# Performance work log

Hardware: AMD Instinct MI355X
Metric: run time of the kernel (lower is better)

Reference implementation:

```python
import jax, jax.numpy as jnp
import numpy as np

EPS = 1e-5

def conv2d(x, w, pad):
    # x: NCHW, w: OIHW, stride 1, symmetric padding
    return jax.lax.conv_general_dilated(
        x, w, window_strides=(1, 1), padding=[(pad, pad), (pad, pad)],
        dimension_numbers=('NCHW', 'OIHW', 'NCHW'))

def bn_eval(x, gamma, beta, mean, var):
    # eval-mode BatchNorm2d: per-channel affine with running stats
    s = gamma / jnp.sqrt(var + EPS)
    return x * s[None, :, None, None] + (beta - mean * s)[None, :, None, None]

def setup_inputs() -> dict:
    key = jax.random.key(0)
    ks = jax.random.split(key, 12)
    B, Cin, C, H, W = 2, 6, 64, 512, 512
    R, K = 4, 5                 # res_num, ksize
    Cf = 2 * 3 * K              # ch_out_final = 30
    d = {}
    d['feature_map'] = jax.random.normal(ks[0], (B, Cin, H, W), jnp.float32)
    d['base'] = jax.random.normal(ks[1], (B, 3, H, W), jnp.float32)
    d['w_first'] = jax.random.normal(ks[2], (C, Cin, 7, 7), jnp.float32) * 0.05
    d['kb_w1'] = jax.random.normal(ks[3], (R, C, C, 3, 3), jnp.float32) * 0.05
    d['kb_g1'] = jnp.ones((R, C), jnp.float32)
    d['kb_b1'] = jnp.zeros((R, C), jnp.float32)
    d['kb_m1'] = jax.random.normal(ks[4], (R, C), jnp.float32) * 0.1
    d['kb_v1'] = jax.random.uniform(ks[5], (R, C), jnp.float32) + 0.5
    d['kb_w2'] = jax.random.normal(ks[6], (R, C, C, 3, 3), jnp.float32) * 0.05
    d['kb_g2'] = jnp.ones((R, C), jnp.float32)
    d['kb_b2'] = jnp.zeros((R, C), jnp.float32)
    d['kb_m2'] = jax.random.normal(ks[7], (R, C), jnp.float32) * 0.1
    d['kb_v2'] = jax.random.uniform(ks[8], (R, C), jnp.float32) + 0.5
    d['w_last'] = jax.random.normal(ks[9], (Cf, C, 3, 3), jnp.float32) * 0.05
    return d

def reference(feature_map, base, w_first, kb_w1, kb_g1, kb_b1, kb_m1, kb_v1,
              kb_w2, kb_g2, kb_b2, kb_m2, kb_v2, w_last):
    K = 5
    P = K // 2
    b, _, h, w = base.shape
    # conv_first: 7x7 conv + ReLU
    y = jax.nn.relu(conv2d(feature_map, w_first, 3))
    # residual KB blocks: (conv3x3 -> BN -> ReLU) x2 + skip
    R = kb_w1.shape[0]
    for i in range(R):
        t = jax.nn.relu(bn_eval(conv2d(y, kb_w1[i], 1), kb_g1[i], kb_b1[i], kb_m1[i], kb_v1[i]))
        t = jax.nn.relu(bn_eval(conv2d(t, kb_w2[i], 1), kb_g2[i], kb_b2[i], kb_m2[i], kb_v2[i]))
        y = t + y
    # conv_last: [b, 2*3*K, h, w]
    y = conv2d(y, w_last, 1)
    Cf = y.shape[1]
    # [b,3,2K,h,w] -> [b,3,h,w,2K]
    weight = y.reshape(b, 3, Cf // 3, h, w).transpose(0, 1, 3, 4, 2)
    weight_h = jax.nn.softmax(weight[..., :K], axis=-1)  # [b,3,h,w,K]
    weight_w = jax.nn.softmax(weight[..., K:], axis=-1)
    # vertical adaptive filtering: pad H by P, unfold along H
    pad_h = jnp.pad(base, ((0, 0), (0, 0), (P, P), (0, 0)))
    unf_h = jnp.stack([pad_h[:, :, i:i + h, :] for i in range(K)], axis=-1)  # [b,3,h,w,K]
    filt_h = (unf_h * weight_h).sum(axis=-1)  # [b,3,h,w]
    # horizontal adaptive filtering: pad W by P, unfold along W
    pad_w = jnp.pad(filt_h, ((0, 0), (0, 0), (0, 0), (P, P)))
    unf_w = jnp.stack([pad_w[:, :, :, i:i + w] for i in range(K)], axis=-1)  # [b,3,h,w,K]
    return (unf_w * weight_w).sum(axis=-1)
```

## Files before the change

kernel.cpp:

```cpp
#include <hip/hip_runtime.h>
#include <math.h>

typedef __attribute__((ext_vector_type(8)))  short short8;
typedef __attribute__((ext_vector_type(4)))  float float4v;
typedef __attribute__((ext_vector_type(16))) float f32x16;

__device__ __forceinline__ unsigned short f2bf(float f) {
    union { float f; unsigned u; } x; x.f = f;
    unsigned r = x.u + 0x7FFFu + ((x.u >> 16) & 1u);
    return (unsigned short)(r >> 16);
}
__device__ __forceinline__ float bf2f(unsigned short u) {
    union { unsigned u; float f; } x; x.u = ((unsigned)u) << 16;
    return x.f;
}

#define HWSZ ((size_t)512 * 512)

__global__ __launch_bounds__(256)
void prep7_k(const float* __restrict__ in, unsigned short* __restrict__ hi,
             unsigned short* __restrict__ lo)
{
    const int idx = blockIdx.x * 256 + threadIdx.x;
    const int b = idx >> 18, rem = idx & 262143;
    const int h = rem >> 9, w = rem & 511;
    unsigned short vh[8], vl[8];
#pragma unroll
    for (int c = 0; c < 8; ++c) {
        float x = (c < 6) ? in[((size_t)(b * 6 + c)) * HWSZ + (h << 9) + w] : 0.f;
        unsigned short h16 = f2bf(x);
        vh[c] = h16;
        vl[c] = f2bf(x - bf2f(h16));
    }
    const size_t o = ((size_t)idx) * 8;
    *(uint4*)(hi + o) = *(uint4*)vh;
    *(uint4*)(lo + o) = *(uint4*)vl;
}

__global__ __launch_bounds__(256)
void repack7_k(const float* __restrict__ wsrc, unsigned short* __restrict__ dhi,
               unsigned short* __restrict__ dlo)
{
    const int t = blockIdx.x * 256 + threadIdx.x;
    if (t >= 26624) return;
    const int j = t & 7, l = (t >> 3) & 63, ct = (t >> 9) & 3, kk = t >> 11;
    const int co = ct * 16 + (l & 15);
    const int s = kk * 4 + (l >> 4);
    float v = 0.f;
    if (s < 49 && j < 6)
        v = wsrc[((size_t)(co * 6 + j) * 7 + s / 7) * 7 + s % 7];
    unsigned short h16 = f2bf(v);
    dhi[t] = h16;
    dlo[t] = f2bf(v - bf2f(h16));
}

__global__ __launch_bounds__(256)
void conv7_mfma(const unsigned short* __restrict__ inhi,
                const unsigned short* __restrict__ inlo,
                const unsigned short* __restrict__ whi,
                const unsigned short* __restrict__ wlo,
                unsigned short* __restrict__ out)
{
    extern __shared__ char p_lds[];

    const int id = blockIdx.x;
    const int lid = (id & 7) * 256 + (id >> 3);
    const int w0 = (lid & 3) * 128;
    const int rest = lid >> 2;
    const int h0 = (rest & 255) * 2;
    const int b  = rest >> 8;

    const int tid = threadIdx.x;
    const int wv = tid >> 6, l = tid & 63, lq = l >> 4, lr = l & 15;

    for (int idx = tid; idx < 2144; idx += 256) {
        const int plane = idx >= 1072;
        const int rc = plane ? idx - 1072 : idx;
        const int r = rc / 134, c = rc % 134;
        const int hh = h0 - 3 + r, wc = w0 - 3 + c;
        int4 v = make_int4(0, 0, 0, 0);
        if (hh >= 0 && hh < 512 && wc >= 0 && wc < 512) {
            const unsigned short* src = plane ? inlo : inhi;
            v = *(const int4*)(src + ((((size_t)b * 512 + hh) * 512) + wc) * 8);
        }
        *(int4*)(p_lds + (size_t)idx * 16) = v;
    }
    __syncthreads();

    float4v acc[2][2][4];
#pragma unroll
    for (int pr = 0; pr < 2; ++pr)
#pragma unroll
        for (int pb = 0; pb < 2; ++pb)
#pragma unroll
            for (int ct = 0; ct < 4; ++ct)
                acc[pr][pb][ct] = (float4v){0.f, 0.f, 0.f, 0.f};

    const int cbase = wv * 32 + lr;
#pragma unroll
    for (int kk = 0; kk < 13; ++kk) {
        int s = kk * 4 + lq;
        if (s > 48) s = 48;
        const int dh = s / 7, dwd = s % 7;
        short8 ah[2][2], al[2][2];
#pragma unroll
        for (int pr = 0; pr < 2; ++pr)
#pragma unroll
            for (int pb = 0; pb < 2; ++pb) {
                const int off = ((pr + dh) * 134 + cbase + pb * 16 + dwd) * 16;
                ah[pr][pb] = *(const short8*)(p_lds + off);
                al[pr][pb] = *(const short8*)(p_lds + 17152 + off);
            }
#pragma unroll
        for (int ct = 0; ct < 4; ++ct) {
            const short8 bh = *(const short8*)(whi + ((size_t)(kk * 4 + ct) * 64 + l) * 8);
            const short8 bl = *(const short8*)(wlo + ((size_t)(kk * 4 + ct) * 64 + l) * 8);
#pragma unroll
            for (int pr = 0; pr < 2; ++pr)
#pragma unroll
                for (int pb = 0; pb < 2; ++pb) {
                    acc[pr][pb][ct] = __builtin_amdgcn_mfma_f32_16x16x32_bf16(ah[pr][pb], bh, acc[pr][pb][ct], 0, 0, 0);
                    acc[pr][pb][ct] = __builtin_amdgcn_mfma_f32_16x16x32_bf16(al[pr][pb], bh, acc[pr][pb][ct], 0, 0, 0);
                    acc[pr][pb][ct] = __builtin_amdgcn_mfma_f32_16x16x32_bf16(ah[pr][pb], bl, acc[pr][pb][ct], 0, 0, 0);
                }
        }
    }

#pragma unroll
    for (int pr = 0; pr < 2; ++pr) {
        const int h = h0 + pr;
#pragma unroll
        for (int pb = 0; pb < 2; ++pb) {
            const int col0 = w0 + wv * 32 + pb * 16 + lq * 4;
#pragma unroll
            for (int ct = 0; ct < 4; ++ct) {
                const int half = ct >> 1, colocal = (ct & 1) * 16 + lr;
#pragma unroll
                for (int rg = 0; rg < 4; ++rg) {
                    const size_t o = ((((size_t)(b * 2 + half) * 512 + h) * 512) + (col0 + rg)) * 32 + colocal;
                    out[o] = f2bf(fmaxf(acc[pr][pb][ct][rg], 0.f));
                }
            }
        }
    }
}

__global__ __launch_bounds__(256)
void repack3n_k(const float* __restrict__ w1, const float* __restrict__ w2,
                const float* __restrict__ g1, const float* __restrict__ v1,
                const float* __restrict__ g2, const float* __restrict__ v2,
                unsigned short* __restrict__ dst)
{
    const int conv = blockIdx.z;
    const float* src = (conv < 4) ? (w1 + (size_t)conv * 36864) : (w2 + (size_t)(conv - 4) * 36864);
    const float* g = (conv < 4) ? (g1 + conv * 64) : (g2 + (conv - 4) * 64);
    const float* vv = (conv < 4) ? (v1 + conv * 64) : (v2 + (conv - 4) * 64);
    unsigned short* d = dst + (size_t)conv * 36864;

    const int t = blockIdx.x * 256 + threadIdx.x;
    const int j = t & 7, l = (t >> 3) & 63;
    const int rest = t >> 9;
    const int s = rest % 9, m = rest / 9;
    const int ch = m & 1, q = m >> 1;
    const int co = ch * 32 + (l & 31);
    const int ci = q * 16 + (l >> 5) * 8 + j;
    const float sc = g[co] * rsqrtf(vv[co] + 1e-5f);
    d[t] = f2bf(src[((size_t)co * 64 + ci) * 9 + s] * sc);
}

__global__ __launch_bounds__(256)
void bias8_k(const float* __restrict__ g1, const float* __restrict__ b1,
             const float* __restrict__ m1, const float* __restrict__ v1,
             const float* __restrict__ g2, const float* __restrict__ b2,
             const float* __restrict__ m2, const float* __restrict__ v2,
             float* __restrict__ bias)
{
    const int t = blockIdx.x * 256 + threadIdx.x;
    if (t >= 512) return;
    const int conv = t >> 6, co = t & 63;
    const float* g = (conv < 4) ? (g1 + conv * 64) : (g2 + (conv - 4) * 64);
    const float* be = (conv < 4) ? (b1 + conv * 64) : (b2 + (conv - 4) * 64);
    const float* mn = (conv < 4) ? (m1 + conv * 64) : (m2 + (conv - 4) * 64);
    const float* vv = (conv < 4) ? (v1 + conv * 64) : (v2 + (conv - 4) * 64);
    const float sc = g[co] * rsqrtf(vv[co] + 1e-5f);
    bias[t] = be[co] - mn[co] * sc;
}

template <bool ADD_>
__global__ __launch_bounds__(256)
void conv3_mfma32(const unsigned short* __restrict__ in,
                  const unsigned short* __restrict__ wrp,
                  const float* __restrict__ bias,
                  const unsigned short* __restrict__ skip,
                  unsigned short* __restrict__ out)
{
    extern __shared__ char smem[];
    char* w_lds = smem;
    char* p_lds = smem + 18432;

    const int id = blockIdx.x;
    const int lid = (id & 7) * 256 + (id >> 3);
    const int w0 = (lid & 3) * 128;
    const int h0 = ((lid >> 2) & 255) * 2;
    const int b  = lid >> 10;

    const int tid = threadIdx.x;
    const int wv = tid >> 6, l = tid & 63;
    const int rw = wv >> 1, tq = wv & 1;
    const int lo5 = l & 31, hi = l >> 5;

    f32x16 acc[2][2];
#pragma unroll
    for (int ch = 0; ch < 2; ++ch)
#pragma unroll
        for (int t4 = 0; t4 < 2; ++t4)
#pragma unroll
            for (int e = 0; e < 16; ++e) acc[ch][t4][e] = 0.f;

    for (int q = 0; q < 4; ++q) {
        if (q) __syncthreads();

        {
            const int4* wsrc = (const int4*)(wrp + (size_t)q * 9216);
            for (int i = tid; i < 1152; i += 256)
                ((int4*)w_lds)[i] = wsrc[i];
        }
        {
            const unsigned short* inp = in + (size_t)(b * 2 + (q >> 1)) * HWSZ * 32;
            const int cbase8 = (q & 1) * 2;
#pragma unroll
            for (int r = 0; r < 4; ++r) {
                const int kg = tid & 1, px = tid >> 1;
                const int hh = h0 - 1 + r, wc = w0 - 1 + px;
                int4 v = make_int4(0, 0, 0, 0);
                if (hh >= 0 && hh < 512 && wc >= 0 && wc < 512)
                    v = *(const int4*)(inp + ((size_t)hh * 512 + wc) * 32 + (cbase8 + kg) * 8);
                *(int4*)(p_lds + ((size_t)((r * 2 + (kg ^ (px & 1))) * 132 + px)) * 16) = v;
            }
            if (tid < 16) {
                const int r = tid >> 2, kg = tid & 1, px = 128 + ((tid >> 1) & 1);
                const int hh = h0 - 1 + r, wc = w0 - 1 + px;
                int4 v = make_int4(0, 0, 0, 0);
                if (hh >= 0 && hh < 512 && wc >= 0 && wc < 512)
                    v = *(const int4*)(inp + ((size_t)hh * 512 + wc) * 32 + (cbase8 + kg) * 8);
                *(int4*)(p_lds + ((size_t)((r * 2 + (kg ^ (px & 1))) * 132 + px)) * 16) = v;
            }
        }
        __syncthreads();

#pragma unroll
        for (int s = 0; s < 9; ++s) {
            const int dh = s / 3, dwd = s % 3;
            const int row = rw + dh;
            short8 pf[2];
#pragma unroll
            for (int t4 = 0; t4 < 2; ++t4) {
                const int px = tq * 64 + t4 * 32 + dwd + lo5;
                pf[t4] = *(const short8*)(p_lds +
                    ((size_t)((row * 2 + (hi ^ (px & 1))) * 132 + px)) * 16);
            }
#pragma unroll
            for (int ch = 0; ch < 2; ++ch) {
                const short8 w8 = *(const short8*)(w_lds +
                    ((size_t)((ch * 9 + s) * 64 + l)) * 16);
#pragma unroll
                for (int t4 = 0; t4 < 2; ++t4)
                    acc[ch][t4] = __builtin_amdgcn_mfma_f32_32x32x16_bf16(
                        pf[t4], w8, acc[ch][t4], 0, 0, 0);
            }
        }
    }

    const int h = h0 + rw;
#pragma unroll
    for (int ch = 0; ch < 2; ++ch) {
        const float bvs = bias[ch * 32 + lo5];
        const size_t pbase = ((size_t)(b * 2 + ch) * HWSZ + (size_t)h * 512);
#pragma unroll
        for (int t4 = 0; t4 < 2; ++t4) {
#pragma unroll
            for (int reg = 0; reg < 16; ++reg) {
                const int pxl = tq * 64 + t4 * 32 + (reg & 3) + 8 * (reg >> 2) + 4 * hi;
                const size_t o = (pbase + (w0 + pxl)) * 32 + lo5;
                float v = fmaxf(acc[ch][t4][reg] + bvs, 0.f);
                if (ADD_) v += bf2f(skip[o]);
                out[o] = f2bf(v);
            }
        }
    }
}

__global__ __launch_bounds__(256)
void repackL_k(const float* __restrict__ wsrc, unsigned short* __restrict__ d)
{
    const int t = blockIdx.x * 256 + threadIdx.x;
    const int j = t & 7, l = (t >> 3) & 63, ct = (t >> 9) & 1, kks = t >> 10;
    const int hf = kks / 9, s = kks % 9;
    const int co = ct * 16 + (l & 15);
    const int ci = hf * 32 + (l >> 4) * 8 + j;
    d[t] = (co < 30) ? f2bf(wsrc[((size_t)co * 64 + ci) * 9 + s]) : (unsigned short)0;
}

template <int NCOT, int OC>
__global__ __launch_bounds__(256)
void conv3_last(const unsigned short* __restrict__ in,
                const unsigned short* __restrict__ wrp,
                unsigned short* __restrict__ out)
{
    extern __shared__ char smem[];
    unsigned short* w_lds = (unsigned short*)smem;
    char* p_lds = smem + NCOT * 9 * 1024;

    const int id = blockIdx.x;
    const int lid = (id & 7) * 256 + (id >> 3);
    const int w0 = (lid & 3) * 128;
    const int rest = lid >> 2;
    const int h0 = (rest & 255) * 2;
    const int b  = rest >> 8;

    const int tid = threadIdx.x;
    const int wv = tid >> 6, l = tid & 63, lq = l >> 4, lr = l & 15;
    const int cbase = wv * 32 + lr;

    float4v acc[2][2][NCOT];
#pragma unroll
    for (int pr = 0; pr < 2; ++pr)
#pragma unroll
        for (int pb = 0; pb < 2; ++pb)
#pragma unroll
            for (int ct = 0; ct < NCOT; ++ct)
                acc[pr][pb][ct] = (float4v){0.f, 0.f, 0.f, 0.f};

    for (int ph = 0; ph < 2; ++ph) {
        const int4* wsrc = (const int4*)(wrp + (size_t)ph * 9 * NCOT * 512);
        for (int i = tid; i < NCOT * 9 * 64; i += 256)
            ((int4*)w_lds)[i] = wsrc[i];
        const unsigned short* inp = in + (size_t)(b * 2 + ph) * HWSZ * 32;
        for (int idx = tid; idx < 2080; idx += 256) {
            const int G = idx & 3, c = (idx >> 2) % 130, rr = idx / 520;
            const int hh = h0 - 1 + rr, wc = w0 - 1 + c;
            int4 v = make_int4(0, 0, 0, 0);
            if (hh >= 0 && hh < 512 && wc >= 0 && wc < 512)
                v = *(const int4*)(inp + ((size_t)hh * 512 + wc) * 32 + G * 8);
            *(int4*)(p_lds + ((size_t)(G * 521 + rr * 130 + c)) * 16) = v;
        }
        __syncthreads();

#pragma unroll
        for (int s = 0; s < 9; ++s) {
            const int dh = s / 3, dwd = s % 3;
            short8 a[2][2];
#pragma unroll
            for (int pr = 0; pr < 2; ++pr)
#pragma unroll
                for (int pb = 0; pb < 2; ++pb)
                    a[pr][pb] = *(const short8*)(p_lds +
                        ((size_t)(lq * 521 + (pr + dh) * 130 + cbase + pb * 16 + dwd)) * 16);
#pragma unroll
            for (int ct = 0; ct < NCOT; ++ct) {
                const short8 bw = *(const short8*)(w_lds + ((size_t)(s * NCOT + ct) * 64 + l) * 8);
#pragma unroll
                for (int pr = 0; pr < 2; ++pr)
#pragma unroll
                    for (int pb = 0; pb < 2; ++pb)
                        acc[pr][pb][ct] = __builtin_amdgcn_mfma_f32_16x16x32_bf16(
                            a[pr][pb], bw, acc[pr][pb][ct], 0, 0, 0);
            }
        }
        __syncthreads();
    }

#pragma unroll
    for (int pr = 0; pr < 2; ++pr) {
        const int h = h0 + pr;
#pragma unroll
        for (int pb = 0; pb < 2; ++pb) {
            const int col0 = w0 + wv * 32 + pb * 16 + lq * 4;
#pragma unroll
            for (int ct = 0; ct < NCOT; ++ct) {
                const int co = ct * 16 + lr;
                if (co < OC) {
#pragma unroll
                    for (int rg = 0; rg < 4; ++rg) {
                        const size_t o = (((size_t)(b * OC + co) * 512 + h) * 512) + (col0 + rg);
                        out[o] = f2bf(acc[pr][pb][ct][rg]);
                    }
                }
            }
        }
    }
}

__global__ __launch_bounds__(256)
void filt_fused_k(const unsigned short* __restrict__ wl, const float* __restrict__ base,
                  float* __restrict__ out)
{
    __shared__ float F[516];

    const int id = blockIdx.x;
    const int lid = (id & 7) * 384 + (id >> 3);
    const int h = lid & 511;
    const int bc = lid >> 9;
    const int b = bc / 3, c = bc % 3;
    const int t = threadIdx.x;

    if (t < 2) F[t] = 0.f;
    if (t >= 254) F[t + 260] = 0.f;

    const size_t rowoff = (size_t)h * 512;
    const unsigned short* wv_p = wl + ((size_t)(b * 30 + c * 10) * HWSZ) + rowoff;
    const unsigned short* wh_p = wv_p + 5 * HWSZ;
    const float* bp = base + (size_t)bc * HWSZ;

#pragma unroll
    for (int wi = 0; wi < 2; ++wi) {
        const int w = t + wi * 256;
        float v[5]; float mx = -1e30f;
#pragma unroll
        for (int i = 0; i < 5; ++i) { v[i] = bf2f(wv_p[(size_t)i * HWSZ + w]); mx = fmaxf(mx, v[i]); }
        float sm = 0.f;
#pragma unroll
        for (int i = 0; i < 5; ++i) { v[i] = __expf(v[i] - mx); sm += v[i]; }
        const float inv = 1.f / sm;
        float acc = 0.f;
#pragma unroll
        for (int i = 0; i < 5; ++i) {
            const int hh = h + i - 2;
            const float bvv = (hh >= 0 && hh < 512) ? bp[(size_t)hh * 512 + w] : 0.f;
            acc = fmaf(bvv, v[i] * inv, acc);
        }
        F[w + 2] = acc;
    }
    __syncthreads();

#pragma unroll
    for (int wi = 0; wi < 2; ++wi) {
        const int w = t + wi * 256;
        float v[5]; float mx = -1e30f;
#pragma unroll
        for (int i = 0; i < 5; ++i) { v[i] = bf2f(wh_p[(size_t)i * HWSZ + w]); mx = fmaxf(mx, v[i]); }
        float sm = 0.f;
#pragma unroll
        for (int i = 0; i < 5; ++i) { v[i] = __expf(v[i] - mx); sm += v[i]; }
        const float inv = 1.f / sm;
        float acc = 0.f;
#pragma unroll
        for (int i = 0; i < 5; ++i)
            acc = fmaf(F[w + i], v[i] * inv, acc);
        out[(size_t)bc * HWSZ + rowoff + w] = acc;
    }
}

extern "C" void kernel_launch(void* const* d_in, const int* in_sizes, int n_in,
                              void* d_out, int out_size, void* d_ws, size_t ws_size,
                              hipStream_t stream)
{
    const float* fm      = (const float*)d_in[0];
    const float* base    = (const float*)d_in[1];
    const float* w_first = (const float*)d_in[2];
    const float* kb_w1   = (const float*)d_in[3];
    const float* kb_g1   = (const float*)d_in[4];
    const float* kb_b1   = (const float*)d_in[5];
    const float* kb_m1   = (const float*)d_in[6];
    const float* kb_v1   = (const float*)d_in[7];
    const float* kb_w2   = (const float*)d_in[8];
    const float* kb_g2   = (const float*)d_in[9];
    const float* kb_b2   = (const float*)d_in[10];
    const float* kb_m2   = (const float*)d_in[11];
    const float* kb_v2   = (const float*)d_in[12];
    const float* w_last  = (const float*)d_in[13];

    char* ws = (char*)d_ws;
    unsigned short* wrp3n  = (unsigned short*)ws;
    unsigned short* wrpL   = wrp3n + (size_t)8 * 36864;
    unsigned short* wrp7hi = wrpL + 18432;
    unsigned short* wrp7lo = wrp7hi + 26624;
    float*          biasws = (float*)(wrp7lo + 26624);
    unsigned short* actA = (unsigned short*)(ws + (1 << 20));
    unsigned short* actB = actA + (size_t)2 * HWSZ * 64;
    unsigned short* actC = actB + (size_t)2 * HWSZ * 64;
    unsigned short* in7hi = actB;
    unsigned short* in7lo = actB + (size_t)2 * HWSZ * 8;
    unsigned short* logits = actC;

    hipFuncSetAttribute((const void*)conv3_mfma32<false>,
                        hipFuncAttributeMaxDynamicSharedMemorySize, 35328);
    hipFuncSetAttribute((const void*)conv3_mfma32<true>,
                        hipFuncAttributeMaxDynamicSharedMemorySize, 35328);
    hipFuncSetAttribute((const void*)conv3_last<2, 30>,
                        hipFuncAttributeMaxDynamicSharedMemorySize, 51776);
    hipFuncSetAttribute((const void*)conv7_mfma,
                        hipFuncAttributeMaxDynamicSharedMemorySize, 34304);

    dim3 blk(256);

    repack3n_k<<<dim3(144, 1, 8), blk, 0, stream>>>(kb_w1, kb_w2, kb_g1, kb_v1, kb_g2, kb_v2, wrp3n);
    bias8_k<<<dim3(2, 1, 1), blk, 0, stream>>>(kb_g1, kb_b1, kb_m1, kb_v1, kb_g2, kb_b2, kb_m2, kb_v2, biasws);
    repackL_k<<<dim3(72, 1, 1), blk, 0, stream>>>(w_last, wrpL);
    repack7_k<<<dim3(104, 1, 1), blk, 0, stream>>>(w_first, wrp7hi, wrp7lo);
    prep7_k<<<dim3(2048, 1, 1), blk, 0, stream>>>(fm, in7hi, in7lo);

    conv7_mfma<<<dim3(2048, 1, 1), blk, 34304, stream>>>(in7hi, in7lo, wrp7hi, wrp7lo, actA);

    unsigned short* cur = actA;
    unsigned short* oth = actC;
    for (int i = 0; i < 4; ++i) {
        conv3_mfma32<false><<<dim3(2048, 1, 1), blk, 35328, stream>>>(
            cur, wrp3n + (size_t)i * 36864, biasws + i * 64, nullptr, actB);
        conv3_mfma32<true><<<dim3(2048, 1, 1), blk, 35328, stream>>>(
            actB, wrp3n + (size_t)(4 + i) * 36864, biasws + (4 + i) * 64, cur, oth);
        unsigned short* t = cur; cur = oth; oth = t;
    }

    conv3_last<2, 30><<<dim3(2048, 1, 1), blk, 51776, stream>>>(cur, wrpL, logits);

    filt_fused_k<<<dim3(3072, 1, 1), blk, 0, stream>>>(logits, base, (float*)d_out);
}
```

Baseline: 649.7 us.

## Use direct global-to-LDS loads and taller 4-row tiles in conv3 MFMA kernel

```diff
diff --git a/kernel.cpp b/kernel.cpp
--- a/kernel.cpp
+++ b/kernel.cpp
@@ -4,6 +4,7 @@
 typedef __attribute__((ext_vector_type(8)))  short short8;
 typedef __attribute__((ext_vector_type(4)))  float float4v;
 typedef __attribute__((ext_vector_type(16))) float f32x16;
+typedef unsigned int u32;
 
 __device__ __forceinline__ unsigned short f2bf(float f) {
     union { float f; unsigned u; } x; x.f = f;
@@ -13,6 +14,12 @@
 __device__ __forceinline__ float bf2f(unsigned short u) {
     union { unsigned u; float f; } x; x.u = ((unsigned)u) << 16;
     return x.f;
+}
+
+__device__ __forceinline__ void gload16(const void* g, void* l) {
+    __builtin_amdgcn_global_load_lds(
+        (const __attribute__((address_space(1))) u32*)g,
+        (__attribute__((address_space(3))) u32*)l, 16, 0, 0);
 }
 
 #define HWSZ ((size_t)512 * 512)
@@ -187,7 +194,7 @@
 }
 
 template <bool ADD_>
-__global__ __launch_bounds__(256)
+__global__ __launch_bounds__(512)
 void conv3_mfma32(const unsigned short* __restrict__ in,
                   const unsigned short* __restrict__ wrp,
                   const float* __restrict__ bias,
@@ -199,10 +206,10 @@
     char* p_lds = smem + 18432;
 
     const int id = blockIdx.x;
-    const int lid = (id & 7) * 256 + (id >> 3);
+    const int lid = (id & 7) * 128 + (id >> 3);
     const int w0 = (lid & 3) * 128;
-    const int h0 = ((lid >> 2) & 255) * 2;
-    const int b  = lid >> 10;
+    const int h0 = ((lid >> 2) & 127) * 4;
+    const int b  = lid >> 9;
 
     const int tid = threadIdx.x;
     const int wv = tid >> 6, l = tid & 63;
@@ -220,31 +227,38 @@
     for (int q = 0; q < 4; ++q) {
         if (q) __syncthreads();
 
-        {
-            const int4* wsrc = (const int4*)(wrp + (size_t)q * 9216);
-            for (int i = tid; i < 1152; i += 256)
-                ((int4*)w_lds)[i] = wsrc[i];
-        }
-        {
-            const unsigned short* inp = in + (size_t)(b * 2 + (q >> 1)) * HWSZ * 32;
-            const int cbase8 = (q & 1) * 2;
-#pragma unroll
-            for (int r = 0; r < 4; ++r) {
-                const int kg = tid & 1, px = tid >> 1;
-                const int hh = h0 - 1 + r, wc = w0 - 1 + px;
-                int4 v = make_int4(0, 0, 0, 0);
-                if (hh >= 0 && hh < 512 && wc >= 0 && wc < 512)
-                    v = *(const int4*)(inp + ((size_t)hh * 512 + wc) * 32 + (cbase8 + kg) * 8);
-                *(int4*)(p_lds + ((size_t)((r * 2 + (kg ^ (px & 1))) * 132 + px)) * 16) = v;
-            }
-            if (tid < 16) {
-                const int r = tid >> 2, kg = tid & 1, px = 128 + ((tid >> 1) & 1);
-                const int hh = h0 - 1 + r, wc = w0 - 1 + px;
-                int4 v = make_int4(0, 0, 0, 0);
-                if (hh >= 0 && hh < 512 && wc >= 0 && wc < 512)
-                    v = *(const int4*)(inp + ((size_t)hh * 512 + wc) * 32 + (cbase8 + kg) * 8);
-                *(int4*)(p_lds + ((size_t)((r * 2 + (kg ^ (px & 1))) * 132 + px)) * 16) = v;
-            }
+        const unsigned short* wq  = wrp + (size_t)q * 9216;
+        const unsigned short* inp = in + (size_t)(b * 2 + (q >> 1)) * HWSZ * 32;
+        const int cb8 = (q & 1) * 2;
+
+        for (int i = wv; i < 42; i += 8) {
+            if (i < 18) {
+                gload16(wq + (size_t)i * 512 + l * 8, w_lds + (size_t)i * 1024);
+            } else {
+                const int j2 = i - 18, p = j2 >> 1, half = j2 & 1;
+                const int row = p >> 1, kg = p & 1;
+                const int hh = h0 - 1 + row;
+                if (hh >= 0 && hh < 512)
+                    gload16(inp + ((size_t)hh * 512 + w0 + half * 64 + l) * 32 + (cb8 + kg) * 8,
+                            p_lds + (size_t)(p * 132 + 1 + half * 64) * 16);
+            }
+        }
+        if (tid < 24) {
+            const int p = tid >> 1, side = tid & 1;
+            const int row = p >> 1, kg = p & 1;
+            const int hh = h0 - 1 + row;
+            const int wc = side ? (w0 + 128) : (w0 - 1);
+            int4 v = make_int4(0, 0, 0, 0);
+            if (hh >= 0 && hh < 512 && wc >= 0 && wc < 512)
+                v = *(const int4*)(inp + ((size_t)hh * 512 + wc) * 32 + (cb8 + kg) * 8);
+            *(int4*)(p_lds + (size_t)(p * 132 + (side ? 129 : 0)) * 16) = v;
+        }
+        if (h0 == 0) {
+            for (int g = tid; g < 264; g += 512)
+                *(int4*)(p_lds + (size_t)g * 16) = make_int4(0, 0, 0, 0);
+        } else if (h0 == 508) {
+            for (int g = tid; g < 264; g += 512)
+                *(int4*)(p_lds + (size_t)(10 * 132 + g) * 16) = make_int4(0, 0, 0, 0);
         }
         __syncthreads();
 
@@ -257,7 +271,7 @@
             for (int t4 = 0; t4 < 2; ++t4) {
                 const int px = tq * 64 + t4 * 32 + dwd + lo5;
                 pf[t4] = *(const short8*)(p_lds +
-                    ((size_t)((row * 2 + (hi ^ (px & 1))) * 132 + px)) * 16);
+                    ((size_t)((row * 2 + hi) * 132 + px)) * 16);
             }
 #pragma unroll
             for (int ch = 0; ch < 2; ++ch) {
@@ -484,9 +498,9 @@
     unsigned short* logits = actC;
 
     hipFuncSetAttribute((const void*)conv3_mfma32<false>,
-                        hipFuncAttributeMaxDynamicSharedMemorySize, 35328);
+                        hipFuncAttributeMaxDynamicSharedMemorySize, 43776);
     hipFuncSetAttribute((const void*)conv3_mfma32<true>,
-                        hipFuncAttributeMaxDynamicSharedMemorySize, 35328);
+                        hipFuncAttributeMaxDynamicSharedMemorySize, 43776);
     hipFuncSetAttribute((const void*)conv3_last<2, 30>,
                         hipFuncAttributeMaxDynamicSharedMemorySize, 51776);
     hipFuncSetAttribute((const void*)conv7_mfma,
@@ -505,9 +519,9 @@
     unsigned short* cur = actA;
     unsigned short* oth = actC;
     for (int i = 0; i < 4; ++i) {
-        conv3_mfma32<false><<<dim3(2048, 1, 1), blk, 35328, stream>>>(
+        conv3_mfma32<false><<<dim3(1024, 1, 1), dim3(512), 43776, stream>>>(
             cur, wrp3n + (size_t)i * 36864, biasws + i * 64, nullptr, actB);
-        conv3_mfma32<true><<<dim3(2048, 1, 1), blk, 35328, stream>>>(
+        conv3_mfma32<true><<<dim3(1024, 1, 1), dim3(512), 43776, stream>>>(
             actB, wrp3n + (size_t)(4 + i) * 36864, biasws + (4 + i) * 64, cur, oth);
         unsigned short* t = cur; cur = oth; oth = t;
     }
```

Measured after the change: 552.5 us. -15.0%, faster.
